# Kernel tuning notes

Hardware: AMD Instinct MI355X
Metric: run time of the kernel (lower is better)

Reference implementation:

```python
import jax, jax.numpy as jnp
import numpy as np

B, N, H, E, M = 2, 20000, 256, 160000, 512


def setup_inputs() -> dict:
    key = jax.random.key(0)
    ks = jax.random.split(key, 8)
    s = 0.02  # small init scale like trained nets
    return {
        "h": jax.random.normal(ks[0], (B, N, H), jnp.float32),
        "edge_index": jax.random.randint(ks[1], (2, E), 0, N, jnp.int64),
        "msg_w1": jax.random.normal(ks[2], (2 * H, M), jnp.float32) * s,
        "msg_b1": jnp.zeros((M,), jnp.float32),
        "msg_w2": jax.random.normal(ks[3], (M, H), jnp.float32) * s,
        "msg_b2": jnp.zeros((H,), jnp.float32),
        "upd_w1": jax.random.normal(ks[4], (2 * H, M), jnp.float32) * s,
        "upd_b1": jnp.zeros((M,), jnp.float32),
        "upd_w2": jax.random.normal(ks[5], (M, H), jnp.float32) * s,
        "upd_b2": jnp.zeros((H,), jnp.float32),
    }


def _mlp(x, w1, b1, w2, b2):
    return jax.nn.relu(x @ w1 + b1) @ w2 + b2


def reference(h, edge_index, msg_w1, msg_b1, msg_w2, msg_b2,
              upd_w1, upd_b1, upd_w2, upd_b2):
    src, dst = edge_index[0], edge_index[1]
    h_src = h[:, src, :]                         # [B,E,H] gather
    h_dst = h[:, dst, :]                         # [B,E,H] gather
    m = _mlp(jnp.concatenate([h_src, h_dst], axis=-1),
             msg_w1, msg_b1, msg_w2, msg_b2)     # [B,E,H]
    agg = jnp.zeros_like(h).at[:, dst, :].add(m) # scatter-add over dst
    upd = _mlp(jnp.concatenate([h, agg], axis=-1),
               upd_w1, upd_b1, upd_w2, upd_b2)   # [B,N,H]
    return h + upd  # mp_residual=True
```

## Files before the change

kernel.cpp:

```cpp
#include <hip/hip_runtime.h>
#include <hip/hip_bf16.h>
#include <stdint.h>

#define B_ 2
#define N_ 20000
#define H_ 256
#define E_ 160000
#define M_ 512

typedef short bf16x8 __attribute__((ext_vector_type(8)));
typedef float f32x4 __attribute__((ext_vector_type(4)));

__device__ __forceinline__ unsigned short f2bf(float f) {
    union { float f; unsigned u; } cv; cv.f = f;
    unsigned u = cv.u;
    unsigned r = u + 0x7fffu + ((u >> 16) & 1u);
    return (unsigned short)(r >> 16);
}
__device__ __forceinline__ unsigned pack2(float a, float b) {
    return (unsigned)f2bf(a) | ((unsigned)f2bf(b) << 16);
}
__device__ __forceinline__ float bflo(unsigned p) {
    union { unsigned u; float f; } c; c.u = p << 16; return c.f;
}

__device__ __forceinline__ void conv_t_one(const float* __restrict__ W,
                                           unsigned short* __restrict__ Wt,
                                           int K, int Ncol, int idx) {
    int n = idx % Ncol;
    int kc = (idx / Ncol) << 3;
    unsigned short t[8];
#pragma unroll
    for (int j = 0; j < 8; ++j) t[j] = f2bf(W[(size_t)(kc + j) * Ncol + n]);
    uint4 v;
    v.x = (unsigned)t[0] | ((unsigned)t[1] << 16);
    v.y = (unsigned)t[2] | ((unsigned)t[3] << 16);
    v.z = (unsigned)t[4] | ((unsigned)t[5] << 16);
    v.w = (unsigned)t[6] | ((unsigned)t[7] << 16);
    *(uint4*)(Wt + (size_t)n * K + kc) = v;
}

__device__ __forceinline__ void conv_w1pq_one(const float* __restrict__ W,
                                              unsigned short* __restrict__ Wt, int idx) {
    int jj = idx & 1023;
    int kc = (idx >> 10) << 3;
    int koff = (jj >= 512) ? 256 : 0;
    int j = jj & 511;
    unsigned short t[8];
#pragma unroll
    for (int r = 0; r < 8; ++r) t[r] = f2bf(W[(size_t)(kc + r + koff) * 512 + j]);
    uint4 v;
    v.x = (unsigned)t[0] | ((unsigned)t[1] << 16);
    v.y = (unsigned)t[2] | ((unsigned)t[3] << 16);
    v.z = (unsigned)t[4] | ((unsigned)t[5] << 16);
    v.w = (unsigned)t[6] | ((unsigned)t[7] << 16);
    *(uint4*)(Wt + (size_t)jj * 256 + kc) = v;
}

__global__ void conv_all(const float* __restrict__ mw1, const float* __restrict__ mw2,
                         const float* __restrict__ uw1, const float* __restrict__ uw2,
                         unsigned short* __restrict__ w1pq, unsigned short* __restrict__ w2t,
                         unsigned short* __restrict__ u1t, unsigned short* __restrict__ u2t) {
    int idx = blockIdx.x * blockDim.x + threadIdx.x;
    if (idx < 32768) {
        conv_w1pq_one(mw1, w1pq, idx);
    } else if (idx < 49152) {
        conv_t_one(mw2, w2t, 512, 256, idx - 32768);
    } else if (idx < 81920) {
        conv_t_one(uw1, u1t, 512, 512, idx - 49152);
    } else if (idx < 98304) {
        conv_t_one(uw2, u2t, 512, 256, idx - 81920);
    }
}

__global__ void hist_kernel(const int* __restrict__ eidx, int* __restrict__ cnt) {
    for (int e = blockIdx.x * blockDim.x + threadIdx.x; e < E_;
         e += gridDim.x * blockDim.x)
        atomicAdd(cnt + eidx[E_ + e], 1);
}

__global__ void scan_kernel(const int* __restrict__ cnt, int* __restrict__ offs,
                            int* __restrict__ cursor) {
    __shared__ int part[1024];
    int t = threadIdx.x;
    int base_i = t * 20;
    int loc[20];
    int s = 0;
#pragma unroll 20
    for (int i = 0; i < 20; ++i) {
        int idx = base_i + i;
        int v = (idx < N_) ? cnt[idx] : 0;
        loc[i] = s;
        s += v;
    }
    part[t] = s;
    __syncthreads();
    for (int off = 1; off < 1024; off <<= 1) {
        int tmp = (t >= off) ? part[t - off] : 0;
        __syncthreads();
        if (t >= off) part[t] += tmp;
        __syncthreads();
    }
    int base = part[t] - s;
#pragma unroll 20
    for (int i = 0; i < 20; ++i) {
        int idx = base_i + i;
        if (idx < N_) {
            int o = base + loc[i];
            offs[idx] = o;
            cursor[idx] = o;
        }
    }
    if (t == 1023) offs[N_] = part[1023];
}

__global__ void scatter_kernel(const int* __restrict__ eidx, int* __restrict__ cursor,
                               int* __restrict__ srcs) {
    for (int e = blockIdx.x * blockDim.x + threadIdx.x; e < E_;
         e += gridDim.x * blockDim.x) {
        int d = eidx[E_ + e];
        int pos = atomicAdd(cursor + d, 1);
        srcs[pos] = eidx[e];
    }
}

__global__ __launch_bounds__(512, 4) void pq_gemm(
    const float* __restrict__ hb,
    const unsigned short* __restrict__ W1pq,
    unsigned short* __restrict__ PQ) {
    __shared__ char smem[64 * 512];
    const int tid = threadIdx.x;
    const int tile = blockIdx.x >> 1;
    const int qh = blockIdx.x & 1;
    const int row0 = tile * 64;

#pragma unroll
    for (int it = 0; it < 8; ++it) {
        int linear = it * 512 + tid;
        int row = linear >> 6;
        int c4 = linear & 63;
        int grow = row0 + row;
        if (grow >= N_) grow = N_ - 1;
        float4 v = *(const float4*)(hb + (size_t)grow * H_ + c4 * 4);
        int byte = (row * 512 + c4 * 8) ^ ((row & 7) << 4);
        uint2 p;
        p.x = pack2(v.x, v.y);
        p.y = pack2(v.z, v.w);
        *(uint2*)(smem + byte) = p;
    }
    __syncthreads();

    const int lane = tid & 63;
    const int w = tid >> 6;
    const int lo = lane & 15;
    const int hi = lane >> 4;
    const int colw = qh * 512 + w * 64;

    f32x4 acc[4][4];
#pragma unroll
    for (int i = 0; i < 4; ++i)
#pragma unroll
        for (int j = 0; j < 4; ++j) acc[i][j] = (f32x4){0.f, 0.f, 0.f, 0.f};

#pragma unroll
    for (int ks = 0; ks < 256; ks += 32) {
        bf16x8 af[4];
#pragma unroll
        for (int rf = 0; rf < 4; ++rf) {
            int row = rf * 16 + lo;
            int byte = (row * 512 + (ks + 8 * hi) * 2) ^ ((row & 7) << 4);
            af[rf] = *(const bf16x8*)(smem + byte);
        }
#pragma unroll
        for (int cf = 0; cf < 4; ++cf) {
            bf16x8 bfr = *(const bf16x8*)(W1pq + (size_t)(colw + cf * 16 + lo) * 256 + ks + 8 * hi);
#pragma unroll
            for (int rf = 0; rf < 4; ++rf)
                acc[rf][cf] = __builtin_amdgcn_mfma_f32_16x16x32_bf16(af[rf], bfr, acc[rf][cf], 0, 0, 0);
        }
    }

#pragma unroll
    for (int cf = 0; cf < 4; ++cf) {
        int col = colw + cf * 16 + lo;
#pragma unroll
        for (int rf = 0; rf < 4; ++rf) {
#pragma unroll
            for (int r = 0; r < 4; ++r) {
                int row = rf * 16 + hi * 4 + r;
                if (row0 + row < N_)
                    PQ[(size_t)(row0 + row) * 1024 + col] = f2bf(acc[rf][cf][r]);
            }
        }
    }
}

__global__ __launch_bounds__(512, 4) void aggupd_kernel(
    const unsigned short* __restrict__ PQ,
    const int* __restrict__ srcs,
    const int* __restrict__ offs,
    const int* __restrict__ cnt,
    const unsigned short* __restrict__ w2t,
    const float* __restrict__ mb1,
    const float* __restrict__ mb2,
    const unsigned short* __restrict__ u1t,
    const float* __restrict__ ub1,
    const unsigned short* __restrict__ u2t,
    const float* __restrict__ ub2,
    const float* __restrict__ hb,
    float* __restrict__ outb) {
    __shared__ char smA[64 * 1024];
    __shared__ int s_cnt[64];

    const int tid = threadIdx.x;
    const int d0 = blockIdx.x * 64;

    if (tid < 64) {
        int dd = d0 + tid;
        s_cnt[tid] = (dd < N_) ? cnt[dd] : 0;
    }

#pragma unroll
    for (int it = 0; it < 8; ++it) {
        int linear = it * 512 + tid;
        int row = linear >> 6;
        int c8 = linear & 63;
        int dd = d0 + row;
        if (dd >= N_) dd = N_ - 1;
        bf16x8 qv = *(const bf16x8*)(PQ + (size_t)dd * 1024 + 512 + c8 * 8);
        const float* bsrc = mb1 + c8 * 8;
        uint4 v;
        float q0, q1;
        q0 = bflo((unsigned)(unsigned short)qv[0]) + bsrc[0];
        q1 = bflo((unsigned)(unsigned short)qv[1]) + bsrc[1];
        v.x = pack2(q0, q1);
        q0 = bflo((unsigned)(unsigned short)qv[2]) + bsrc[2];
        q1 = bflo((unsigned)(unsigned short)qv[3]) + bsrc[3];
        v.y = pack2(q0, q1);
        q0 = bflo((unsigned)(unsigned short)qv[4]) + bsrc[4];
        q1 = bflo((unsigned)(unsigned short)qv[5]) + bsrc[5];
        v.z = pack2(q0, q1);
        q0 = bflo((unsigned)(unsigned short)qv[6]) + bsrc[6];
        q1 = bflo((unsigned)(unsigned short)qv[7]) + bsrc[7];
        v.w = pack2(q0, q1);
        int byte = (row * 1024 + c8 * 16) ^ ((row & 7) << 4);
        *(uint4*)(smA + byte) = v;
    }
    __syncthreads();

    const int dsub = tid >> 3;
    const int part = tid & 7;
    {
        const int d = d0 + dsub;
        int beg = 0, end = 0;
        if (d < N_) { beg = offs[d]; end = offs[d + 1]; }

        float acc[64];
#pragma unroll
        for (int i = 0; i < 64; ++i) acc[i] = 0.f;

        int p = beg;
        for (; p + 1 < end; p += 2) {
            int s0 = srcs[p];
            int s1 = srcs[p + 1];
            const unsigned short* r0 = PQ + (size_t)s0 * 1024;
            const unsigned short* r1 = PQ + (size_t)s1 * 1024;
#pragma unroll
            for (int half = 0; half < 2; ++half) {
                bf16x8 v0[4], v1[4];
#pragma unroll
                for (int c = 0; c < 4; ++c) {
                    int ch = half * 4 + c;
                    v0[c] = *(const bf16x8*)(r0 + (ch * 8 + part) * 8);
                    v1[c] = *(const bf16x8*)(r1 + (ch * 8 + part) * 8);
                }
#pragma unroll
                for (int c = 0; c < 4; ++c) {
                    int ch = half * 4 + c;
                    int byte = (dsub * 1024 + (ch * 8 + part) * 16) ^ ((dsub & 7) << 4);
                    bf16x8 qv = *(const bf16x8*)(smA + byte);
#pragma unroll
                    for (int j = 0; j < 8; ++j) {
                        float q = bflo((unsigned)(unsigned short)qv[j]);
                        acc[ch * 8 + j] += fmaxf(bflo((unsigned)(unsigned short)v0[c][j]) + q, 0.f)
                                         + fmaxf(bflo((unsigned)(unsigned short)v1[c][j]) + q, 0.f);
                    }
                }
            }
        }
        if (p < end) {
            int s0 = srcs[p];
            const unsigned short* r0 = PQ + (size_t)s0 * 1024;
#pragma unroll
            for (int half = 0; half < 2; ++half) {
                bf16x8 v0[4];
#pragma unroll
                for (int c = 0; c < 4; ++c) {
                    int ch = half * 4 + c;
                    v0[c] = *(const bf16x8*)(r0 + (ch * 8 + part) * 8);
                }
#pragma unroll
                for (int c = 0; c < 4; ++c) {
                    int ch = half * 4 + c;
                    int byte = (dsub * 1024 + (ch * 8 + part) * 16) ^ ((dsub & 7) << 4);
                    bf16x8 qv = *(const bf16x8*)(smA + byte);
#pragma unroll
                    for (int j = 0; j < 8; ++j) {
                        float q = bflo((unsigned)(unsigned short)qv[j]);
                        acc[ch * 8 + j] += fmaxf(bflo((unsigned)(unsigned short)v0[c][j]) + q, 0.f);
                    }
                }
            }
        }
        __syncthreads();

#pragma unroll
        for (int c = 0; c < 8; ++c) {
            uint4 v;
            v.x = pack2(acc[c * 8 + 0], acc[c * 8 + 1]);
            v.y = pack2(acc[c * 8 + 2], acc[c * 8 + 3]);
            v.z = pack2(acc[c * 8 + 4], acc[c * 8 + 5]);
            v.w = pack2(acc[c * 8 + 6], acc[c * 8 + 7]);
            int byte = (dsub * 1024 + (c * 8 + part) * 16) ^ ((dsub & 7) << 4);
            *(uint4*)(smA + byte) = v;
        }
    }
    __syncthreads();

    const int lane = tid & 63;
    const int w = tid >> 6;
    const int lo = lane & 15;
    const int hi = lane >> 4;

    f32x4 aB[4][2];
#pragma unroll
    for (int i = 0; i < 4; ++i)
#pragma unroll
        for (int j = 0; j < 2; ++j) aB[i][j] = (f32x4){0.f, 0.f, 0.f, 0.f};
    {
        const int colw = w * 32;
        for (int ks = 0; ks < 512; ks += 32) {
            bf16x8 af[4];
#pragma unroll
            for (int rf = 0; rf < 4; ++rf) {
                int row = rf * 16 + lo;
                int byte = (row * 1024 + (ks + 8 * hi) * 2) ^ ((row & 7) << 4);
                af[rf] = *(const bf16x8*)(smA + byte);
            }
#pragma unroll
            for (int cf = 0; cf < 2; ++cf) {
                bf16x8 bfr = *(const bf16x8*)(w2t + (size_t)(colw + cf * 16 + lo) * 512 + ks + 8 * hi);
#pragma unroll
                for (int rf = 0; rf < 4; ++rf)
                    aB[rf][cf] = __builtin_amdgcn_mfma_f32_16x16x32_bf16(af[rf], bfr, aB[rf][cf], 0, 0, 0);
            }
        }
    }
    __syncthreads();

#pragma unroll
    for (int it = 0; it < 4; ++it) {
        int linear = it * 512 + tid;
        int row = linear >> 5;
        int c8 = linear & 31;
        int grow = d0 + row;
        if (grow >= N_) grow = N_ - 1;
        const float* src = hb + (size_t)grow * H_ + c8 * 8;
        float4 a = *(const float4*)src;
        float4 b = *(const float4*)(src + 4);
        uint4 v;
        v.x = pack2(a.x, a.y);
        v.y = pack2(a.z, a.w);
        v.z = pack2(b.x, b.y);
        v.w = pack2(b.z, b.w);
        int byte = (row * 1024 + c8 * 16) ^ ((row & 7) << 4);
        *(uint4*)(smA + byte) = v;
    }
    {
        const int colw = w * 32;
#pragma unroll
        for (int cf = 0; cf < 2; ++cf) {
            int col = colw + cf * 16 + lo;
            float bb = mb2[col];
#pragma unroll
            for (int rf = 0; rf < 4; ++rf) {
#pragma unroll
                for (int r = 0; r < 4; ++r) {
                    int row = rf * 16 + hi * 4 + r;
                    float v = aB[rf][cf][r] + (float)s_cnt[row] * bb;
                    int byte = (row * 1024 + (256 + col) * 2) ^ ((row & 7) << 4);
                    *(unsigned short*)(smA + byte) = f2bf(v);
                }
            }
        }
    }
    __syncthreads();

    f32x4 aC[4][4];
#pragma unroll
    for (int i = 0; i < 4; ++i)
#pragma unroll
        for (int j = 0; j < 4; ++j) aC[i][j] = (f32x4){0.f, 0.f, 0.f, 0.f};
    {
        const int colw = w * 64;
        for (int ks = 0; ks < 512; ks += 32) {
            bf16x8 af[4];
#pragma unroll
            for (int rf = 0; rf < 4; ++rf) {
                int row = rf * 16 + lo;
                int byte = (row * 1024 + (ks + 8 * hi) * 2) ^ ((row & 7) << 4);
                af[rf] = *(const bf16x8*)(smA + byte);
            }
#pragma unroll
            for (int cf = 0; cf < 4; ++cf) {
                bf16x8 bfr = *(const bf16x8*)(u1t + (size_t)(colw + cf * 16 + lo) * 512 + ks + 8 * hi);
#pragma unroll
                for (int rf = 0; rf < 4; ++rf)
                    aC[rf][cf] = __builtin_amdgcn_mfma_f32_16x16x32_bf16(af[rf], bfr, aC[rf][cf], 0, 0, 0);
            }
        }
    }
    __syncthreads();

    {
        const int colw = w * 64;
#pragma unroll
        for (int cf = 0; cf < 4; ++cf) {
            int col = colw + cf * 16 + lo;
            float bb = ub1[col];
#pragma unroll
            for (int rf = 0; rf < 4; ++rf) {
#pragma unroll
                for (int r = 0; r < 4; ++r) {
                    float v = fmaxf(aC[rf][cf][r] + bb, 0.f);
                    int row = rf * 16 + hi * 4 + r;
                    int byte = (row * 1024 + col * 2) ^ ((row & 7) << 4);
                    *(unsigned short*)(smA + byte) = f2bf(v);
                }
            }
        }
    }
    __syncthreads();

    {
        const int colw = w * 32;
        f32x4 aD[4][2];
#pragma unroll
        for (int i = 0; i < 4; ++i)
#pragma unroll
            for (int j = 0; j < 2; ++j) aD[i][j] = (f32x4){0.f, 0.f, 0.f, 0.f};

        for (int ks = 0; ks < 512; ks += 32) {
            bf16x8 af[4];
#pragma unroll
            for (int rf = 0; rf < 4; ++rf) {
                int row = rf * 16 + lo;
                int byte = (row * 1024 + (ks + 8 * hi) * 2) ^ ((row & 7) << 4);
                af[rf] = *(const bf16x8*)(smA + byte);
            }
#pragma unroll
            for (int cf = 0; cf < 2; ++cf) {
                bf16x8 bfr = *(const bf16x8*)(u2t + (size_t)(colw + cf * 16 + lo) * 512 + ks + 8 * hi);
#pragma unroll
                for (int rf = 0; rf < 4; ++rf)
                    aD[rf][cf] = __builtin_amdgcn_mfma_f32_16x16x32_bf16(af[rf], bfr, aD[rf][cf], 0, 0, 0);
            }
        }

#pragma unroll
        for (int cf = 0; cf < 2; ++cf) {
            int col = colw + cf * 16 + lo;
            float bb = ub2[col];
#pragma unroll
            for (int rf = 0; rf < 4; ++rf) {
#pragma unroll
                for (int r = 0; r < 4; ++r) {
                    int row = rf * 16 + hi * 4 + r;
                    int grow = d0 + row;
                    if (grow < N_) {
                        size_t o = (size_t)grow * H_ + col;
                        outb[o] = hb[o] + aD[rf][cf][r] + bb;
                    }
                }
            }
        }
    }
}

extern "C" void kernel_launch(void* const* d_in, const int* in_sizes, int n_in,
                              void* d_out, int out_size, void* d_ws, size_t ws_size,
                              hipStream_t stream) {
    const float* h      = (const float*)d_in[0];
    const int*   eidx   = (const int*)d_in[1];
    const float* msg_w1 = (const float*)d_in[2];
    const float* msg_b1 = (const float*)d_in[3];
    const float* msg_w2 = (const float*)d_in[4];
    const float* msg_b2 = (const float*)d_in[5];
    const float* upd_w1 = (const float*)d_in[6];
    const float* upd_b1 = (const float*)d_in[7];
    const float* upd_w2 = (const float*)d_in[8];
    const float* upd_b2 = (const float*)d_in[9];
    float* out = (float*)d_out;

    char* ws = (char*)d_ws;
    size_t off = 0;
    auto alloc = [&](size_t bytes) {
        char* p = ws + off;
        off = (off + bytes + 255) & ~(size_t)255;
        return p;
    };
    unsigned short* PQ   = (unsigned short*)alloc((size_t)N_ * 1024 * 2);
    unsigned short* w1pq = (unsigned short*)alloc(1024 * 256 * 2);
    unsigned short* w2t  = (unsigned short*)alloc(256 * 512 * 2);
    unsigned short* u1t  = (unsigned short*)alloc(512 * 512 * 2);
    unsigned short* u2t  = (unsigned short*)alloc(256 * 512 * 2);
    int* cnt    = (int*)alloc(N_ * 4);
    int* offs   = (int*)alloc((N_ + 1) * 4);
    int* cursor = (int*)alloc(N_ * 4);
    int* srcs   = (int*)alloc(E_ * 4);
    if (ws_size < off) return;

    hipMemsetAsync(cnt, 0, N_ * 4, stream);
    conv_all<<<384, 256, 0, stream>>>(msg_w1, msg_w2, upd_w1, upd_w2, w1pq, w2t, u1t, u2t);

    hist_kernel<<<256, 256, 0, stream>>>(eidx, cnt);
    scan_kernel<<<1, 1024, 0, stream>>>(cnt, offs, cursor);
    scatter_kernel<<<256, 256, 0, stream>>>(eidx, cursor, srcs);

    const int nblk = (N_ + 63) / 64;
    for (int b = 0; b < B_; ++b) {
        const float* hb = h + (size_t)b * N_ * H_;
        pq_gemm<<<nblk * 2, 512, 0, stream>>>(hb, w1pq, PQ);
        aggupd_kernel<<<nblk, 512, 0, stream>>>(PQ, srcs, offs, cnt, w2t,
                                                msg_b1, msg_b2,
                                                u1t, upd_b1, u2t, upd_b2,
                                                hb, out + (size_t)b * N_ * H_);
    }
}
```

Measured before the change: 502.4 us.

## Split edge gather-aggregate into separate wave-per-node kernel before MLP

Moves the per-destination gather of P rows plus ReLU summation out of the fused aggregate/update kernel into its own kernel. Each wave handles one destination node across all 512 channels, unrolled over four edges, and writes the summed hidden activations to a new bf16 workspace buffer. The MLP kernel then just loads that buffer into shared memory. This removes the 64-float accumulator register pressure and the 8-threads-per-node layout from the GEMM kernel, giving more memory-level parallelism for the random gathers. The cost is an extra global write and read of a 20000x512 bf16 buffer and an extra launch per batch.

```diff
diff --git a/kernel.cpp b/kernel.cpp
--- a/kernel.cpp
+++ b/kernel.cpp
@@ -195,13 +195,72 @@
     }
 }
 
-__global__ __launch_bounds__(512, 4) void aggupd_kernel(
+__global__ __launch_bounds__(256, 8) void gather_kernel(
     const unsigned short* __restrict__ PQ,
     const int* __restrict__ srcs,
     const int* __restrict__ offs,
+    const float* __restrict__ mb1,
+    unsigned short* __restrict__ hsum) {
+    const int lane = threadIdx.x & 63;
+    const int nw = (gridDim.x * blockDim.x) >> 6;
+    const int wid0 = (blockIdx.x * blockDim.x + threadIdx.x) >> 6;
+
+    float bq[8];
+#pragma unroll
+    for (int j = 0; j < 8; ++j) bq[j] = mb1[lane * 8 + j];
+
+    for (int d = wid0; d < N_; d += nw) {
+        bf16x8 qv = *(const bf16x8*)(PQ + (size_t)d * 1024 + 512 + lane * 8);
+        float qb[8];
+#pragma unroll
+        for (int j = 0; j < 8; ++j)
+            qb[j] = bflo((unsigned)(unsigned short)qv[j]) + bq[j];
+
+        float acc[8];
+#pragma unroll
+        for (int j = 0; j < 8; ++j) acc[j] = 0.f;
+
+        int p = offs[d];
+        const int end = offs[d + 1];
+        for (; p + 3 < end; p += 4) {
+            int s0 = srcs[p];
+            int s1 = srcs[p + 1];
+            int s2 = srcs[p + 2];
+            int s3 = srcs[p + 3];
+            bf16x8 v0 = *(const bf16x8*)(PQ + (size_t)s0 * 1024 + lane * 8);
+            bf16x8 v1 = *(const bf16x8*)(PQ + (size_t)s1 * 1024 + lane * 8);
+            bf16x8 v2 = *(const bf16x8*)(PQ + (size_t)s2 * 1024 + lane * 8);
+            bf16x8 v3 = *(const bf16x8*)(PQ + (size_t)s3 * 1024 + lane * 8);
+#pragma unroll
+            for (int j = 0; j < 8; ++j) {
+                float q = qb[j];
+                acc[j] += fmaxf(bflo((unsigned)(unsigned short)v0[j]) + q, 0.f)
+                        + fmaxf(bflo((unsigned)(unsigned short)v1[j]) + q, 0.f)
+                        + fmaxf(bflo((unsigned)(unsigned short)v2[j]) + q, 0.f)
+                        + fmaxf(bflo((unsigned)(unsigned short)v3[j]) + q, 0.f);
+            }
+        }
+        for (; p < end; ++p) {
+            int s0 = srcs[p];
+            bf16x8 v0 = *(const bf16x8*)(PQ + (size_t)s0 * 1024 + lane * 8);
+#pragma unroll
+            for (int j = 0; j < 8; ++j)
+                acc[j] += fmaxf(bflo((unsigned)(unsigned short)v0[j]) + qb[j], 0.f);
+        }
+
+        uint4 v;
+        v.x = pack2(acc[0], acc[1]);
+        v.y = pack2(acc[2], acc[3]);
+        v.z = pack2(acc[4], acc[5]);
+        v.w = pack2(acc[6], acc[7]);
+        *(uint4*)(hsum + (size_t)d * 512 + lane * 8) = v;
+    }
+}
+
+__global__ __launch_bounds__(512, 4) void mlp_kernel(
+    const unsigned short* __restrict__ hsum,
     const int* __restrict__ cnt,
     const unsigned short* __restrict__ w2t,
-    const float* __restrict__ mb1,
     const float* __restrict__ mb2,
     const unsigned short* __restrict__ u1t,
     const float* __restrict__ ub1,
@@ -227,103 +286,9 @@
         int c8 = linear & 63;
         int dd = d0 + row;
         if (dd >= N_) dd = N_ - 1;
-        bf16x8 qv = *(const bf16x8*)(PQ + (size_t)dd * 1024 + 512 + c8 * 8);
-        const float* bsrc = mb1 + c8 * 8;
-        uint4 v;
-        float q0, q1;
-        q0 = bflo((unsigned)(unsigned short)qv[0]) + bsrc[0];
-        q1 = bflo((unsigned)(unsigned short)qv[1]) + bsrc[1];
-        v.x = pack2(q0, q1);
-        q0 = bflo((unsigned)(unsigned short)qv[2]) + bsrc[2];
-        q1 = bflo((unsigned)(unsigned short)qv[3]) + bsrc[3];
-        v.y = pack2(q0, q1);
-        q0 = bflo((unsigned)(unsigned short)qv[4]) + bsrc[4];
-        q1 = bflo((unsigned)(unsigned short)qv[5]) + bsrc[5];
-        v.z = pack2(q0, q1);
-        q0 = bflo((unsigned)(unsigned short)qv[6]) + bsrc[6];
-        q1 = bflo((unsigned)(unsigned short)qv[7]) + bsrc[7];
-        v.w = pack2(q0, q1);
+        uint4 v = *(const uint4*)(hsum + (size_t)dd * 512 + c8 * 8);
         int byte = (row * 1024 + c8 * 16) ^ ((row & 7) << 4);
         *(uint4*)(smA + byte) = v;
-    }
-    __syncthreads();
-
-    const int dsub = tid >> 3;
-    const int part = tid & 7;
-    {
-        const int d = d0 + dsub;
-        int beg = 0, end = 0;
-        if (d < N_) { beg = offs[d]; end = offs[d + 1]; }
-
-        float acc[64];
-#pragma unroll
-        for (int i = 0; i < 64; ++i) acc[i] = 0.f;
-
-        int p = beg;
-        for (; p + 1 < end; p += 2) {
-            int s0 = srcs[p];
-            int s1 = srcs[p + 1];
-            const unsigned short* r0 = PQ + (size_t)s0 * 1024;
-            const unsigned short* r1 = PQ + (size_t)s1 * 1024;
-#pragma unroll
-            for (int half = 0; half < 2; ++half) {
-                bf16x8 v0[4], v1[4];
-#pragma unroll
-                for (int c = 0; c < 4; ++c) {
-                    int ch = half * 4 + c;
-                    v0[c] = *(const bf16x8*)(r0 + (ch * 8 + part) * 8);
-                    v1[c] = *(const bf16x8*)(r1 + (ch * 8 + part) * 8);
-                }
-#pragma unroll
-                for (int c = 0; c < 4; ++c) {
-                    int ch = half * 4 + c;
-                    int byte = (dsub * 1024 + (ch * 8 + part) * 16) ^ ((dsub & 7) << 4);
-                    bf16x8 qv = *(const bf16x8*)(smA + byte);
-#pragma unroll
-                    for (int j = 0; j < 8; ++j) {
-                        float q = bflo((unsigned)(unsigned short)qv[j]);
-                        acc[ch * 8 + j] += fmaxf(bflo((unsigned)(unsigned short)v0[c][j]) + q, 0.f)
-                                         + fmaxf(bflo((unsigned)(unsigned short)v1[c][j]) + q, 0.f);
-                    }
-                }
-            }
-        }
-        if (p < end) {
-            int s0 = srcs[p];
-            const unsigned short* r0 = PQ + (size_t)s0 * 1024;
-#pragma unroll
-            for (int half = 0; half < 2; ++half) {
-                bf16x8 v0[4];
-#pragma unroll
-                for (int c = 0; c < 4; ++c) {
-                    int ch = half * 4 + c;
-                    v0[c] = *(const bf16x8*)(r0 + (ch * 8 + part) * 8);
-                }
-#pragma unroll
-                for (int c = 0; c < 4; ++c) {
-                    int ch = half * 4 + c;
-                    int byte = (dsub * 1024 + (ch * 8 + part) * 16) ^ ((dsub & 7) << 4);
-                    bf16x8 qv = *(const bf16x8*)(smA + byte);
-#pragma unroll
-                    for (int j = 0; j < 8; ++j) {
-                        float q = bflo((unsigned)(unsigned short)qv[j]);
-                        acc[ch * 8 + j] += fmaxf(bflo((unsigned)(unsigned short)v0[c][j]) + q, 0.f);
-                    }
-                }
-            }
-        }
-        __syncthreads();
-
-#pragma unroll
-        for (int c = 0; c < 8; ++c) {
-            uint4 v;
-            v.x = pack2(acc[c * 8 + 0], acc[c * 8 + 1]);
-            v.y = pack2(acc[c * 8 + 2], acc[c * 8 + 3]);
-            v.z = pack2(acc[c * 8 + 4], acc[c * 8 + 5]);
-            v.w = pack2(acc[c * 8 + 6], acc[c * 8 + 7]);
-            int byte = (dsub * 1024 + (c * 8 + part) * 16) ^ ((dsub & 7) << 4);
-            *(uint4*)(smA + byte) = v;
-        }
     }
     __syncthreads();
 
@@ -510,6 +475,7 @@
         return p;
     };
     unsigned short* PQ   = (unsigned short*)alloc((size_t)N_ * 1024 * 2);
+    unsigned short* hsum = (unsigned short*)alloc((size_t)N_ * 512 * 2);
     unsigned short* w1pq = (unsigned short*)alloc(1024 * 256 * 2);
     unsigned short* w2t  = (unsigned short*)alloc(256 * 512 * 2);
     unsigned short* u1t  = (unsigned short*)alloc(512 * 512 * 2);
@@ -531,9 +497,9 @@
     for (int b = 0; b < B_; ++b) {
         const float* hb = h + (size_t)b * N_ * H_;
         pq_gemm<<<nblk * 2, 512, 0, stream>>>(hb, w1pq, PQ);
-        aggupd_kernel<<<nblk, 512, 0, stream>>>(PQ, srcs, offs, cnt, w2t,
-                                                msg_b1, msg_b2,
-                                                u1t, upd_b1, u2t, upd_b2,
-                                                hb, out + (size_t)b * N_ * H_);
-    }
-}
+        gather_kernel<<<2048, 256, 0, stream>>>(PQ, srcs, offs, msg_b1, hsum);
+        mlp_kernel<<<nblk, 512, 0, stream>>>(hsum, cnt, w2t, msg_b2,
+                                             u1t, upd_b1, u2t, upd_b2,
+                                             hb, out + (size_t)b * N_ * H_);
+    }
+}
```

After: 404.3 us. 19.5% less time.
